# Optimization experiments

Measured on AMD Instinct MI355X. Metric: run time of the kernel, lower is better.

Reference implementation:

```python
import jax, jax.numpy as jnp
import numpy as np

D_IN, D_OUT, K = 128, 128, 64
X_MIN, X_MAX = 0.0, 1.0
EPS = 1e-12


def _pchip_slopes(y, x):
    # y: [..., K], x: [K] strictly increasing -> slopes [..., K]. Assumes K >= 3.
    h = x[1:] - x[:-1]                      # [K-1]
    delta = (y[..., 1:] - y[..., :-1]) / (h + EPS)
    h0, h1 = h[:-1], h[1:]
    w1 = 2.0 * h1 + h0
    w2 = h1 + 2.0 * h0
    d0_, d1_ = delta[..., :-1], delta[..., 1:]
    same_sign = d0_ * d1_ > 0
    denom = w1 / (d0_ + EPS) + w2 / (d1_ + EPS)
    d_int = jnp.where(same_sign, (w1 + w2) / (denom + EPS), 0.0)  # [..., K-2]
    d_first = ((2.0 * h[0] + h[1]) * delta[..., 0] - h[0] * delta[..., 1]) / (h[0] + h[1] + EPS)
    d_last = ((2.0 * h[-1] + h[-2]) * delta[..., -1] - h[-1] * delta[..., -2]) / (h[-1] + h[-2] + EPS)

    def limit(di, de):
        di = jnp.where(di * de <= 0, 0.0, di)
        return jnp.where(jnp.abs(di) > 3.0 * jnp.abs(de), 3.0 * de, di)

    d_first = limit(d_first, delta[..., 0])
    d_last = limit(d_last, delta[..., -1])
    return jnp.concatenate([d_first[..., None], d_int, d_last[..., None]], axis=-1)


def setup_inputs() -> dict:
    key = jax.random.key(0)
    k1, k2 = jax.random.split(key)
    x = jax.random.normal(k1, (4096, D_IN), dtype=jnp.float32)
    coeffs = 0.2 * jax.random.normal(k2, (D_OUT, D_IN, K), dtype=jnp.float32)
    bias = jnp.zeros((D_OUT,), dtype=jnp.float32)
    knots = jnp.linspace(X_MIN, X_MAX, K, dtype=jnp.float32)
    return {"x": x, "coeffs": coeffs, "bias": bias, "knots": knots}


def reference(x, coeffs, bias, knots):
    B = x.shape[0]
    slopes = _pchip_slopes(coeffs, knots)              # [d_out, d_in, K]
    h = (X_MAX - X_MIN) / (K - 1)

    xc = jnp.clip(x, X_MIN, X_MAX)                     # [B, d_in]
    idx = jnp.clip(jnp.floor((xc - X_MIN) / h).astype(jnp.int32), 0, K - 2)
    t = (xc - (X_MIN + idx.astype(x.dtype) * h)) / h   # [B, d_in]
    t2 = t * t
    t3 = t2 * t
    h00 = 2 * t3 - 3 * t2 + 1
    h10 = t3 - 2 * t2 + t
    h01 = -2 * t3 + 3 * t2
    h11 = t3 - t2

    ct = jnp.transpose(coeffs, (1, 2, 0))              # [d_in, K, d_out]
    dt = jnp.transpose(slopes, (1, 2, 0))              # [d_in, K, d_out]
    ii = jnp.arange(D_IN)[None, :]                     # [1, d_in]
    y0 = ct[ii, idx]                                   # [B, d_in, d_out]
    y1 = ct[ii, idx + 1]
    d0 = dt[ii, idx]
    d1 = dt[ii, idx + 1]

    yi = (h00[..., None] * y0 + h10[..., None] * h * d0
          + h01[..., None] * y1 + h11[..., None] * h * d1)  # [B, d_in, d_out]

    # linear extrapolation beyond the knot range
    y_left = ct[:, 0, :][None] + dt[:, 0, :][None] * (x - X_MIN)[..., None]
    y_right = ct[:, -1, :][None] + dt[:, -1, :][None] * (x - X_MAX)[..., None]
    yi = jnp.where((x < X_MIN)[..., None], y_left, yi)
    yi = jnp.where((x > X_MAX)[..., None], y_right, yi)

    return yi.sum(axis=1) + bias[None, :]              # [B, d_out]
```

## Files before the change

kernel.cpp:

```cpp
#include <hip/hip_runtime.h>

#define KN 64
#define DIN 128
#define DOUT 128
#define NJ 63
#define EPSF 1e-12f


__global__ __launch_bounds__(256) void kan_precompute(
    const float* __restrict__ coeffs,
    const float* __restrict__ knots,
    float4* __restrict__ pk)
{
    const int wave = threadIdx.x >> 6;
    const int lane = threadIdx.x & 63;
    const int i = blockIdx.x & 127;
    const int o = ((blockIdx.x >> 7) << 2) + wave;

    float y  = coeffs[(o * DIN + i) * KN + lane];
    float kn  = knots[lane];
    float kn1 = (lane < 63) ? knots[lane + 1] : 0.0f;
    float hk  = kn1 - kn;

    float ynext = __shfl_down(y, 1);
    float delta = (lane < 63) ? (ynext - y) / (hk + EPSF) : 0.0f;

    float dm1 = __shfl_up(delta, 1);
    float hm1 = __shfl_up(hk, 1);

    float w1v = 2.0f * hk + hm1;
    float w2v = hk + 2.0f * hm1;
    float denom = w1v / (dm1 + EPSF) + w2v / (delta + EPSF);
    float d = (dm1 * delta > 0.0f) ? (w1v + w2v) / (denom + EPSF) : 0.0f;

    float d1v = __shfl_down(delta, 1);
    float h1v = __shfl_down(hk, 1);
    if (lane == 0) {
        float df = ((2.0f * hk + h1v) * delta - hk * d1v) / (hk + h1v + EPSF);
        if (df * delta <= 0.0f) df = 0.0f;
        else if (fabsf(df) > 3.0f * fabsf(delta)) df = 3.0f * delta;
        d = df;
    }
    float dm2 = __shfl_up(delta, 2);
    float hm2 = __shfl_up(hk, 2);
    if (lane == 63) {
        float dl = ((2.0f * hm1 + hm2) * dm1 - hm1 * dm2) / (hm1 + hm2 + EPSF);
        if (dl * dm1 <= 0.0f) dl = 0.0f;
        else if (fabsf(dl) > 3.0f * fabsf(dm1)) dl = 3.0f * dm1;
        d = dl;
    }

    float ynx = __shfl_down(y, 1);
    float dnx = __shfl_down(d, 1);
    if (lane < NJ) {
        pk[(i * NJ + lane) * DOUT + o] = make_float4(y, d, ynx, dnx);
    }
}

__global__ __launch_bounds__(128) void kan_main(
    const float* __restrict__ x,
    const float4* __restrict__ pk,
    const float* __restrict__ bias,
    float* __restrict__ out)
{
    const int b = blockIdx.x;
    const int o = threadIdx.x;

    __shared__ float4 wts[DIN];
    __shared__ int    idxs[DIN];

    const float h = 1.0f / 63.0f;

    float xv = x[b * DIN + o];
    float xc = fminf(fmaxf(xv, 0.0f), 1.0f);
    int idx = (int)floorf(xc / h);
    idx = idx < 0 ? 0 : (idx > 62 ? 62 : idx);
    float t = (xc - (float)idx * h) / h;
    float t2 = t * t, t3 = t2 * t;
    float w0 = 2.0f * t3 - 3.0f * t2 + 1.0f;
    float w1 = (t3 - 2.0f * t2 + t) * h;
    float w2 = 3.0f * t2 - 2.0f * t3;
    float w3 = (t3 - t2) * h;
    if (xv < 0.0f)      { w0 = 1.0f; w1 = xv;        w2 = 0.0f; w3 = 0.0f;      idx = 0;  }
    else if (xv > 1.0f) { w0 = 0.0f; w1 = 0.0f;      w2 = 1.0f; w3 = xv - 1.0f; idx = 62; }
    wts[o]  = make_float4(w0, w1, w2, w3);
    idxs[o] = idx;
    __syncthreads();

    float acc0 = 0.0f, acc1 = 0.0f, acc2 = 0.0f, acc3 = 0.0f;
    #pragma unroll 4
    for (int i = 0; i < DIN; i += 4) {
        float4 wA = wts[i];     int jA = idxs[i];
        float4 wB = wts[i + 1]; int jB = idxs[i + 1];
        float4 wC = wts[i + 2]; int jC = idxs[i + 2];
        float4 wD = wts[i + 3]; int jD = idxs[i + 3];
        float4 fA = pk[((i    ) * NJ + jA) * DOUT + o];
        float4 fB = pk[((i + 1) * NJ + jB) * DOUT + o];
        float4 fC = pk[((i + 2) * NJ + jC) * DOUT + o];
        float4 fD = pk[((i + 3) * NJ + jD) * DOUT + o];
        acc0 += wA.x * fA.x + wA.y * fA.y + wA.z * fA.z + wA.w * fA.w;
        acc1 += wB.x * fB.x + wB.y * fB.y + wB.z * fB.z + wB.w * fB.w;
        acc2 += wC.x * fC.x + wC.y * fC.y + wC.z * fC.z + wC.w * fC.w;
        acc3 += wD.x * fD.x + wD.y * fD.y + wD.z * fD.z + wD.w * fD.w;
    }

    out[b * DOUT + o] = acc0 + acc1 + acc2 + acc3 + bias[o];
}

extern "C" void kernel_launch(void* const* d_in, const int* in_sizes, int n_in,
                              void* d_out, int out_size, void* d_ws, size_t ws_size,
                              hipStream_t stream) {
    const float* x      = (const float*)d_in[0];
    const float* coeffs = (const float*)d_in[1];
    const float* bias   = (const float*)d_in[2];
    const float* knots  = (const float*)d_in[3];
    float* out = (float*)d_out;
    float4* pk = (float4*)d_ws;

    kan_precompute<<<4096, 256, 0, stream>>>(coeffs, knots, pk);
    kan_main<<<4096, 128, 0, stream>>>(x, pk, bias, out);
}
```

Baseline: 109.4 us.

## Pack spline table as fp16 pairs with coalesced precompute via shared memory

The precomputed per-segment table shrinks from float4 to four fp16 values (y, scaled slope), halving the bytes gathered in the main kernel. The precompute kernel is restructured so each block handles 64 outputs for one input: slopes are staged in padded shared memory, then written transposed so stores to the table are coalesced. The slope is prescaled by h so the main kernel's weights lose the h factor. This trades fp16 rounding of coefficients and slopes for lower memory traffic, which risks failing accuracy tolerance.

```diff
diff --git a/kernel.cpp b/kernel.cpp
--- a/kernel.cpp
+++ b/kernel.cpp
@@ -1,65 +1,80 @@
 #include <hip/hip_runtime.h>
+#include <hip/hip_fp16.h>
 
 #define KN 64
 #define DIN 128
 #define DOUT 128
 #define NJ 63
 #define EPSF 1e-12f
+#define HF (1.0f / 63.0f)
 
 
 __global__ __launch_bounds__(256) void kan_precompute(
     const float* __restrict__ coeffs,
     const float* __restrict__ knots,
-    float4* __restrict__ pk)
+    uint2* __restrict__ pk)
 {
-    const int wave = threadIdx.x >> 6;
-    const int lane = threadIdx.x & 63;
-    const int i = blockIdx.x & 127;
-    const int o = ((blockIdx.x >> 7) << 2) + wave;
+    const int i      = blockIdx.x >> 1;
+    const int o_base = (blockIdx.x & 1) << 6;
+    const int wave   = threadIdx.x >> 6;
+    const int lane   = threadIdx.x & 63;
 
-    float y  = coeffs[(o * DIN + i) * KN + lane];
+    __shared__ float ys[64][65];
+    __shared__ float ds[64][65];
+
     float kn  = knots[lane];
     float kn1 = (lane < 63) ? knots[lane + 1] : 0.0f;
     float hk  = kn1 - kn;
+    float hm1 = __shfl_up(hk, 1);
+    float h1v = __shfl_down(hk, 1);
+    float hm2 = __shfl_up(hk, 2);
 
-    float ynext = __shfl_down(y, 1);
-    float delta = (lane < 63) ? (ynext - y) / (hk + EPSF) : 0.0f;
+    for (int ol = wave; ol < 64; ol += 4) {
+        const int o = o_base + ol;
+        float y = coeffs[(o * DIN + i) * KN + lane];
+        float ynext = __shfl_down(y, 1);
+        float delta = (lane < 63) ? (ynext - y) / (hk + EPSF) : 0.0f;
+        float dm1 = __shfl_up(delta, 1);
 
-    float dm1 = __shfl_up(delta, 1);
-    float hm1 = __shfl_up(hk, 1);
+        float w1v = 2.0f * hk + hm1;
+        float w2v = hk + 2.0f * hm1;
+        float denom = w1v / (dm1 + EPSF) + w2v / (delta + EPSF);
+        float d = (dm1 * delta > 0.0f) ? (w1v + w2v) / (denom + EPSF) : 0.0f;
 
-    float w1v = 2.0f * hk + hm1;
-    float w2v = hk + 2.0f * hm1;
-    float denom = w1v / (dm1 + EPSF) + w2v / (delta + EPSF);
-    float d = (dm1 * delta > 0.0f) ? (w1v + w2v) / (denom + EPSF) : 0.0f;
+        float d1v = __shfl_down(delta, 1);
+        if (lane == 0) {
+            float df = ((2.0f * hk + h1v) * delta - hk * d1v) / (hk + h1v + EPSF);
+            if (df * delta <= 0.0f) df = 0.0f;
+            else if (fabsf(df) > 3.0f * fabsf(delta)) df = 3.0f * delta;
+            d = df;
+        }
+        float dm2 = __shfl_up(delta, 2);
+        if (lane == 63) {
+            float dl = ((2.0f * hm1 + hm2) * dm1 - hm1 * dm2) / (hm1 + hm2 + EPSF);
+            if (dl * dm1 <= 0.0f) dl = 0.0f;
+            else if (fabsf(dl) > 3.0f * fabsf(dm1)) dl = 3.0f * dm1;
+            d = dl;
+        }
+        ys[ol][lane] = y;
+        ds[ol][lane] = d * HF;
+    }
+    __syncthreads();
 
-    float d1v = __shfl_down(delta, 1);
-    float h1v = __shfl_down(hk, 1);
-    if (lane == 0) {
-        float df = ((2.0f * hk + h1v) * delta - hk * d1v) / (hk + h1v + EPSF);
-        if (df * delta <= 0.0f) df = 0.0f;
-        else if (fabsf(df) > 3.0f * fabsf(delta)) df = 3.0f * delta;
-        d = df;
-    }
-    float dm2 = __shfl_up(delta, 2);
-    float hm2 = __shfl_up(hk, 2);
-    if (lane == 63) {
-        float dl = ((2.0f * hm1 + hm2) * dm1 - hm1 * dm2) / (hm1 + hm2 + EPSF);
-        if (dl * dm1 <= 0.0f) dl = 0.0f;
-        else if (fabsf(dl) > 3.0f * fabsf(dm1)) dl = 3.0f * dm1;
-        d = dl;
-    }
-
-    float ynx = __shfl_down(y, 1);
-    float dnx = __shfl_down(d, 1);
-    if (lane < NJ) {
-        pk[(i * NJ + lane) * DOUT + o] = make_float4(y, d, ynx, dnx);
+    const int ol = threadIdx.x & 63;
+    const int jb = threadIdx.x >> 6;
+    for (int j = jb; j < NJ; j += 4) {
+        __half2 p0 = __floats2half2_rn(ys[ol][j],     ds[ol][j]);
+        __half2 p1 = __floats2half2_rn(ys[ol][j + 1], ds[ol][j + 1]);
+        uint2 v;
+        v.x = *reinterpret_cast<unsigned int*>(&p0);
+        v.y = *reinterpret_cast<unsigned int*>(&p1);
+        pk[(i * NJ + j) * DOUT + o_base + ol] = v;
     }
 }
 
 __global__ __launch_bounds__(128) void kan_main(
     const float* __restrict__ x,
-    const float4* __restrict__ pk,
+    const uint2* __restrict__ pk,
     const float* __restrict__ bias,
     float* __restrict__ out)
 {
@@ -69,7 +84,7 @@
     __shared__ float4 wts[DIN];
     __shared__ int    idxs[DIN];
 
-    const float h = 1.0f / 63.0f;
+    const float h = HF;
 
     float xv = x[b * DIN + o];
     float xc = fminf(fmaxf(xv, 0.0f), 1.0f);
@@ -78,11 +93,11 @@
     float t = (xc - (float)idx * h) / h;
     float t2 = t * t, t3 = t2 * t;
     float w0 = 2.0f * t3 - 3.0f * t2 + 1.0f;
-    float w1 = (t3 - 2.0f * t2 + t) * h;
+    float w1 = t3 - 2.0f * t2 + t;
     float w2 = 3.0f * t2 - 2.0f * t3;
-    float w3 = (t3 - t2) * h;
-    if (xv < 0.0f)      { w0 = 1.0f; w1 = xv;        w2 = 0.0f; w3 = 0.0f;      idx = 0;  }
-    else if (xv > 1.0f) { w0 = 0.0f; w1 = 0.0f;      w2 = 1.0f; w3 = xv - 1.0f; idx = 62; }
+    float w3 = t3 - t2;
+    if (xv < 0.0f)      { w0 = 1.0f; w1 = xv / h;          w2 = 0.0f; w3 = 0.0f;  idx = 0;  }
+    else if (xv > 1.0f) { w0 = 0.0f; w1 = 0.0f; w2 = 1.0f; w3 = (xv - 1.0f) / h;  idx = 62; }
     wts[o]  = make_float4(w0, w1, w2, w3);
     idxs[o] = idx;
     __syncthreads();
@@ -94,14 +109,22 @@
         float4 wB = wts[i + 1]; int jB = idxs[i + 1];
         float4 wC = wts[i + 2]; int jC = idxs[i + 2];
         float4 wD = wts[i + 3]; int jD = idxs[i + 3];
-        float4 fA = pk[((i    ) * NJ + jA) * DOUT + o];
-        float4 fB = pk[((i + 1) * NJ + jB) * DOUT + o];
-        float4 fC = pk[((i + 2) * NJ + jC) * DOUT + o];
-        float4 fD = pk[((i + 3) * NJ + jD) * DOUT + o];
-        acc0 += wA.x * fA.x + wA.y * fA.y + wA.z * fA.z + wA.w * fA.w;
-        acc1 += wB.x * fB.x + wB.y * fB.y + wB.z * fB.z + wB.w * fB.w;
-        acc2 += wC.x * fC.x + wC.y * fC.y + wC.z * fC.z + wC.w * fC.w;
-        acc3 += wD.x * fD.x + wD.y * fD.y + wD.z * fD.z + wD.w * fD.w;
+        uint2 qA = pk[((i    ) * NJ + jA) * DOUT + o];
+        uint2 qB = pk[((i + 1) * NJ + jB) * DOUT + o];
+        uint2 qC = pk[((i + 2) * NJ + jC) * DOUT + o];
+        uint2 qD = pk[((i + 3) * NJ + jD) * DOUT + o];
+        float2 lA = __half22float2(*reinterpret_cast<const __half2*>(&qA.x));
+        float2 hA = __half22float2(*reinterpret_cast<const __half2*>(&qA.y));
+        float2 lB = __half22float2(*reinterpret_cast<const __half2*>(&qB.x));
+        float2 hB = __half22float2(*reinterpret_cast<const __half2*>(&qB.y));
+        float2 lC = __half22float2(*reinterpret_cast<const __half2*>(&qC.x));
+        float2 hC = __half22float2(*reinterpret_cast<const __half2*>(&qC.y));
+        float2 lD = __half22float2(*reinterpret_cast<const __half2*>(&qD.x));
+        float2 hD = __half22float2(*reinterpret_cast<const __half2*>(&qD.y));
+        acc0 += wA.x * lA.x + wA.y * lA.y + wA.z * hA.x + wA.w * hA.y;
+        acc1 += wB.x * lB.x + wB.y * lB.y + wB.z * hB.x + wB.w * hB.y;
+        acc2 += wC.x * lC.x + wC.y * lC.y + wC.z * hC.x + wC.w * hC.y;
+        acc3 += wD.x * lD.x + wD.y * lD.y + wD.z * hD.x + wD.w * hD.y;
     }
 
     out[b * DOUT + o] = acc0 + acc1 + acc2 + acc3 + bias[o];
@@ -115,8 +138,8 @@
     const float* bias   = (const float*)d_in[2];
     const float* knots  = (const float*)d_in[3];
     float* out = (float*)d_out;
-    float4* pk = (float4*)d_ws;
+    uint2* pk = (uint2*)d_ws;
 
-    kan_precompute<<<4096, 256, 0, stream>>>(coeffs, knots, pk);
+    kan_precompute<<<256, 256, 0, stream>>>(coeffs, knots, pk);
     kan_main<<<4096, 128, 0, stream>>>(x, pk, bias, out);
 }
```

After: 110.4 us. About the same (+1.0%).
